# Performance work log

Measured on AMD Instinct MI355X. Metric: run time of the kernel, lower is better.

The kernel has to match this reference:

```python
import jax, jax.numpy as jnp
import numpy as np

QLEN, KLEN, BSZ, NHEAD, DHEAD = 1024, 1024, 2, 16, 64
RLEN = QLEN + KLEN
SCALE = 1.0 / np.sqrt(DHEAD).astype(np.float32)  # 1/sqrt(d_head)


def setup_inputs() -> dict:
    key = jax.random.key(0)
    ks = jax.random.split(key, 10)
    return {
        "q_head": jax.random.normal(ks[0], (QLEN, BSZ, NHEAD, DHEAD), jnp.float32),
        "k_head_h": jax.random.normal(ks[1], (KLEN, BSZ, NHEAD, DHEAD), jnp.float32),
        "v_head_h": jax.random.normal(ks[2], (KLEN, BSZ, NHEAD, DHEAD), jnp.float32),
        "k_head_r": jax.random.normal(ks[3], (RLEN, BSZ, NHEAD, DHEAD), jnp.float32),
        "seg_embed": jax.random.normal(ks[4], (2, NHEAD, DHEAD), jnp.float32),
        "seg_mat": jax.random.uniform(ks[5], (QLEN, KLEN, BSZ, 2), jnp.float32),
        "r_w_bias": jax.random.normal(ks[6], (NHEAD, DHEAD), jnp.float32),
        "r_r_bias": jax.random.normal(ks[7], (NHEAD, DHEAD), jnp.float32),
        "r_s_bias": jax.random.normal(ks[8], (NHEAD, DHEAD), jnp.float32),
        "attn_mask": jnp.zeros((QLEN, KLEN, 1, 1), jnp.float32),
    }


def _rel_shift(x, klen):
    # x: [qlen, rlen, bsz, n_head] -> [qlen, klen, bsz, n_head]
    x = jnp.transpose(x, (1, 0, 2, 3))[1:]          # drop first position row
    x = jnp.transpose(x, (1, 0, 2, 3))[:, :klen]    # keep first klen columns
    return x


def reference(q_head, k_head_h, v_head_h, k_head_r, seg_embed, seg_mat,
              r_w_bias, r_r_bias, r_s_bias, attn_mask):
    # content-based score
    ac = jnp.einsum('ibnd,jbnd->ijbn', q_head + r_w_bias, k_head_h)
    # position-based score with relative shift
    bd = jnp.einsum('ibnd,jbnd->ijbn', q_head + r_r_bias, k_head_r)
    bd = _rel_shift(bd, klen=ac.shape[1])
    # segment-based score
    ef = jnp.einsum('ibnd,snd->ibns', q_head + r_s_bias, seg_embed)
    ef = jnp.einsum('ijbs,ibns->ijbn', seg_mat, ef)
    attn_score = (ac + bd + ef) * SCALE
    attn_score = attn_score - 1e30 * attn_mask
    attn_prob = jax.nn.softmax(attn_score, axis=1)  # over key dim j
    attn_vec = jnp.einsum('ijbn,jbnd->ibnd', attn_prob, v_head_h)
    return attn_vec
```

## Files before the change

kernel.cpp:

```cpp
#include <hip/hip_runtime.h>

#define QLEN 1024
#define KLEN 1024
#define BSZ 2
#define NHEAD 16
#define DHEAD 64
#define RS 2048
#define BLK_I 64
#define BLK_J 32
#define NT32 (KLEN / BLK_J)
#define NBN (BSZ * NHEAD)

#define SC2f  0.18033688011112440f
#define MBIGf 1.4426950408889634e30f

#define SEGP_BYTES  16777216u
#define KT_BYTES    ((size_t)NBN * NT32 * 4096)

typedef __attribute__((ext_vector_type(8))) short s16x8;
typedef __attribute__((ext_vector_type(8))) unsigned short u16x8;
typedef __attribute__((ext_vector_type(4))) unsigned short u16x4;
typedef __attribute__((ext_vector_type(4))) float f32x4;
typedef __attribute__((ext_vector_type(2))) float f32x2;

__device__ __forceinline__ unsigned short f2bf(float f) {
    union { float f; unsigned int u; } x; x.f = f;
    unsigned int r = x.u + 0x7fffu + ((x.u >> 16) & 1u);
    return (unsigned short)(r >> 16);
}
__device__ __forceinline__ float bf2f(unsigned short h) {
    union { unsigned int u; float f; } x; x.u = ((unsigned int)h) << 16;
    return x.f;
}

typedef const __attribute__((address_space(1))) unsigned int* gas_t;
typedef __attribute__((address_space(3))) unsigned int* las_t;
__device__ __forceinline__ void gl_lds16(const void* g, void* l) {
    __builtin_amdgcn_global_load_lds((gas_t)g, (las_t)l, 16, 0, 0);
}

__global__ __launch_bounds__(256)
void pack_all_kernel(const float* __restrict__ segmat,
                     const float* __restrict__ mask,
                     const float* __restrict__ kh,
                     const float* __restrict__ kr,
                     const float* __restrict__ v,
                     u16x4* __restrict__ segP,
                     unsigned short* __restrict__ Kp,
                     unsigned short* __restrict__ Krp,
                     unsigned short* __restrict__ Vtp)
{
    __shared__ float VT[32][65];
    const int bid = blockIdx.x;
    const int tid = threadIdx.x;

    if (bid < 1024) {
        const int gid = bid * 256 + tid;
        const int j8  = gid & (KLEN / 8 - 1);
        const int i   = (gid >> 7) & (QLEN - 1);
        const int b   = gid >> 17;
        const float* sp = segmat + ((size_t)(i * KLEN + j8 * 8) * BSZ + b) * 2;
        const float* mp = mask + (size_t)i * KLEN + j8 * 8;
        u16x4* op = segP + (size_t)(b * QLEN + i) * KLEN + j8 * 8;
#pragma unroll
        for (int e = 0; e < 8; ++e) {
            const f32x2 sm = *(const f32x2*)(sp + e * (BSZ * 2));
            u16x4 pk;
            pk[0] = f2bf(sm[0]); pk[1] = f2bf(sm[1]);
            pk[2] = f2bf(mp[e] * MBIGf); pk[3] = 0;
            op[e] = pk;
        }
    } else {
        const int blk = bid - 1024;
        const int bn  = blk >> 5;
        const int jt  = blk & (NT32 - 1);
        const int b   = bn & 1;
        const int n   = bn >> 1;
        const int boff = b * NHEAD * DHEAD + n * DHEAD;
        const int j0  = jt * BLK_J;

        {
            const int j  = tid >> 3;
            const int dq = (tid & 7) * 8;
            const float* vp = v + (size_t)(j0 + j) * RS + boff + dq;
#pragma unroll
            for (int e = 0; e < 8; ++e) VT[j][dq + e] = vp[e];
        }
        __syncthreads();

        const size_t tb = (size_t)blk * 2048;
        {
            const int row = tid >> 3;
            const int ch  = (tid & 7) ^ (row & 7);
            u16x8 ok, orr;
            const float* hp = kh + (size_t)(j0 + row) * RS + boff + ch * 8;
            const float* rp = kr + (size_t)(j0 + row + 1) * RS + boff + ch * 8;
#pragma unroll
            for (int e = 0; e < 8; ++e) { ok[e] = f2bf(hp[e]); orr[e] = f2bf(rp[e]); }
            *(u16x8*)&Kp [tb + (size_t)tid * 8] = ok;
            *(u16x8*)&Krp[tb + (size_t)tid * 8] = orr;
        }
        {
            const int d  = tid >> 2;
            const int g  = tid & 3;
            const int ch = g ^ (d & 3);
            u16x8 ov;
#pragma unroll
            for (int e = 0; e < 8; ++e) ov[e] = f2bf(VT[ch * 8 + e][d]);
            *(u16x8*)&Vtp[tb + (size_t)tid * 8] = ov;
        }
    }
}

__global__ __launch_bounds__(256, 2)
void relattn_kernel(const float* __restrict__ q,
                    const float* __restrict__ segemb,
                    const float* __restrict__ rwb,
                    const float* __restrict__ rrb,
                    const float* __restrict__ rsb,
                    const u16x4* __restrict__ segP,
                    const unsigned short* __restrict__ Kp,
                    const unsigned short* __restrict__ Krp,
                    const unsigned short* __restrict__ Vtp,
                    float* __restrict__ out)
{
    __shared__ unsigned short KhL[2][32][64];
    __shared__ unsigned short KrL[2][32][64];
    __shared__ unsigned short VtL[2][64][32];
    __shared__ unsigned short PlP[4][16][40];

    const int F = blockIdx.x;
    const int x = F & 7;
    const int k = F >> 3;
    const int g = (k >> 4) * 8 + x;
    const int i0 = (g >> 1) * BLK_I;
    const int b  = g & 1;
    const int n  = k & 15;
    const int bn = n * 2 + b;
    const int boff = b * NHEAD * DHEAD + n * DHEAD;

    const int tid  = threadIdx.x;
    const int wave = tid >> 6;
    const int lane = tid & 63;
    const int q4   = lane >> 4;
    const int c    = lane & 15;
    const int iRow = i0 + wave * 16 + c;

    s16x8 qwf[2], qrf[2];
    float e0, e1;
    {
        const float* qp = q + (size_t)iRow * RS + boff;
        float es0 = 0.f, es1 = 0.f;
#pragma unroll
        for (int kk = 0; kk < 2; ++kk) {
            const int off = kk * 32 + q4 * 8;
            const f32x4 q0 = *(const f32x4*)(qp + off);
            const f32x4 q1 = *(const f32x4*)(qp + off + 4);
            const f32x4 w0 = *(const f32x4*)(rwb + n * DHEAD + off);
            const f32x4 w1 = *(const f32x4*)(rwb + n * DHEAD + off + 4);
            const f32x4 r0 = *(const f32x4*)(rrb + n * DHEAD + off);
            const f32x4 r1 = *(const f32x4*)(rrb + n * DHEAD + off + 4);
            const f32x4 sa = *(const f32x4*)(segemb + n * DHEAD + off);
            const f32x4 sb = *(const f32x4*)(segemb + n * DHEAD + off + 4);
            const f32x4 ta = *(const f32x4*)(segemb + (NHEAD + n) * DHEAD + off);
            const f32x4 tb = *(const f32x4*)(segemb + (NHEAD + n) * DHEAD + off + 4);
            const f32x4 ra = *(const f32x4*)(rsb + n * DHEAD + off);
            const f32x4 rb = *(const f32x4*)(rsb + n * DHEAD + off + 4);
            s16x8 tw, tr;
#pragma unroll
            for (int e = 0; e < 4; ++e) {
                tw[e]     = (short)f2bf(q0[e] + w0[e]);
                tw[4 + e] = (short)f2bf(q1[e] + w1[e]);
                tr[e]     = (short)f2bf(q0[e] + r0[e]);
                tr[4 + e] = (short)f2bf(q1[e] + r1[e]);
                es0 += (q0[e] + ra[e]) * sa[e] + (q1[e] + rb[e]) * sb[e];
                es1 += (q0[e] + ra[e]) * ta[e] + (q1[e] + rb[e]) * tb[e];
            }
            qwf[kk] = tw; qrf[kk] = tr;
        }
        es0 += __shfl_xor(es0, 16, 64); es0 += __shfl_xor(es0, 32, 64);
        es1 += __shfl_xor(es1, 16, 64); es1 += __shfl_xor(es1, 32, 64);
        e0 = es0 * SC2f; e1 = es1 * SC2f;
    }

    const int tbase = bn * NT32;
    auto stage = [&](int jt, int buf) {
        const size_t toff = ((size_t)(tbase + jt)) << 12;
        const int go = tid * 16;
        const int lo = wave * 1024;
        gl_lds16((const char*)Kp  + toff + go, (char*)&KhL[buf][0][0] + lo);
        gl_lds16((const char*)Krp + toff + go, (char*)&KrL[buf][0][0] + lo);
        gl_lds16((const char*)Vtp + toff + go, (char*)&VtL[buf][0][0] + lo);
    };

    stage(0, 0);
    __syncthreads();

    float m = -INFINITY, lsum = 0.f;
    f32x4 acc[4];
#pragma unroll
    for (int dt = 0; dt < 4; ++dt) acc[dt] = (f32x4)0.f;

    const u16x4* spB = segP + (size_t)b * QLEN * KLEN;
    int cur = 0;
    for (int jt = 0; jt < NT32; ++jt) {
        if (jt + 1 < NT32) stage(jt + 1, cur ^ 1);

        const int j0g = jt * BLK_J;
        u16x8 pg[2][2];
        {
            const u16x4* pp = spB + (size_t)iRow * KLEN + j0g + q4 * 4;
            pg[0][0] = *(const u16x8*)pp;
            pg[0][1] = *(const u16x8*)(pp + 2);
            pg[1][0] = *(const u16x8*)(pp + 16);
            pg[1][1] = *(const u16x8*)(pp + 18);
        }

        f32x4 sjT[2];
        sjT[0] = (f32x4)0.f; sjT[1] = (f32x4)0.f;
        __builtin_amdgcn_s_setprio(1);
#pragma unroll
        for (int kk = 0; kk < 2; ++kk)
#pragma unroll
            for (int js = 0; js < 2; ++js) {
                const int row = js * 16 + c;
                const int pcK = ((kk * 4 + q4) ^ (c & 7)) * 8;
                const s16x8 khf = *(const s16x8*)&KhL[cur][row][pcK];
                const s16x8 krf = *(const s16x8*)&KrL[cur][row][pcK];
                sjT[js] = __builtin_amdgcn_mfma_f32_16x16x32_bf16(khf, qwf[kk], sjT[js], 0, 0, 0);
                sjT[js] = __builtin_amdgcn_mfma_f32_16x16x32_bf16(krf, qrf[kk], sjT[js], 0, 0, 0);
            }
        __builtin_amdgcn_s_setprio(0);

        float sc8[8];
#pragma unroll
        for (int js = 0; js < 2; ++js)
#pragma unroll
            for (int r = 0; r < 4; ++r) {
                const u16x8 g2 = pg[js][r >> 1];
                const int bb = (r & 1) * 4;
                sc8[js * 4 + r] = sjT[js][r] * SC2f
                                  + bf2f(g2[bb]) * e0 + bf2f(g2[bb + 1]) * e1
                                  - bf2f(g2[bb + 2]);
            }
        float mt = fmaxf(
            fmaxf(fmaxf(sc8[0], sc8[1]), fmaxf(sc8[2], sc8[3])),
            fmaxf(fmaxf(sc8[4], sc8[5]), fmaxf(sc8[6], sc8[7])));
        mt = fmaxf(mt, __shfl_xor(mt, 16, 64));
        mt = fmaxf(mt, __shfl_xor(mt, 32, 64));
        const float mn  = fmaxf(m, mt);
        const float scl = __builtin_amdgcn_exp2f(m - mn);
        m = mn;
#pragma unroll
        for (int dt = 0; dt < 4; ++dt) acc[dt] *= scl;
        float p[8], ps = 0.f;
#pragma unroll
        for (int e = 0; e < 8; ++e) {
            p[e] = __builtin_amdgcn_exp2f(sc8[e] - m);
            ps += p[e];
        }
        lsum = lsum * scl + ps;

#pragma unroll
        for (int js = 0; js < 2; ++js) {
            unsigned int wlo, whi;
            asm("v_cvt_pk_bf16_f32 %0, %1, %2" : "=v"(wlo) : "v"(p[js * 4 + 0]), "v"(p[js * 4 + 1]));
            asm("v_cvt_pk_bf16_f32 %0, %1, %2" : "=v"(whi) : "v"(p[js * 4 + 2]), "v"(p[js * 4 + 3]));
            uint2 wv; wv.x = wlo; wv.y = whi;
            *(uint2*)((char*)&PlP[wave][c][0] + js * 32 + q4 * 8) = wv;
        }
        const s16x8 pf = *(const s16x8*)&PlP[wave][c][q4 * 8];

        __builtin_amdgcn_s_setprio(1);
#pragma unroll
        for (int dt = 0; dt < 4; ++dt) {
            const s16x8 vf = *(const s16x8*)&VtL[cur][dt * 16 + c][(q4 ^ (c & 3)) * 8];
            acc[dt] = __builtin_amdgcn_mfma_f32_16x16x32_bf16(vf, pf, acc[dt], 0, 0, 0);
        }
        __builtin_amdgcn_s_setprio(0);

        __syncthreads();
        cur ^= 1;
    }

    lsum += __shfl_xor(lsum, 16, 64);
    lsum += __shfl_xor(lsum, 32, 64);

    {
        const float inv = 1.f / lsum;
        float* op = out + (size_t)iRow * RS + boff;
#pragma unroll
        for (int dt = 0; dt < 4; ++dt) {
            const f32x4 o = acc[dt] * inv;
            *(f32x4*)&op[dt * 16 + q4 * 4] = o;
        }
    }
}

extern "C" void kernel_launch(void* const* d_in, const int* in_sizes, int n_in,
                              void* d_out, int out_size, void* d_ws, size_t ws_size,
                              hipStream_t stream) {
    const float* q   = (const float*)d_in[0];
    const float* kh  = (const float*)d_in[1];
    const float* v   = (const float*)d_in[2];
    const float* kr  = (const float*)d_in[3];
    const float* se  = (const float*)d_in[4];
    const float* sm  = (const float*)d_in[5];
    const float* rwb = (const float*)d_in[6];
    const float* rrb = (const float*)d_in[7];
    const float* rsb = (const float*)d_in[8];
    const float* msk = (const float*)d_in[9];
    float* out = (float*)d_out;

    char* wsb = (char*)d_ws;
    u16x4* segP = (u16x4*)wsb;
    unsigned short* Kp  = (unsigned short*)(wsb + SEGP_BYTES);
    unsigned short* Krp = (unsigned short*)(wsb + SEGP_BYTES + KT_BYTES);
    unsigned short* Vtp = (unsigned short*)(wsb + SEGP_BYTES + 2 * KT_BYTES);

    pack_all_kernel<<<1024 + NBN * NT32, 256, 0, stream>>>(sm, msk, kh, kr, v,
                                                           segP, Kp, Krp, Vtp);
    relattn_kernel<<<512, 256, 0, stream>>>(q, se, rwb, rrb, rsb, segP, Kp, Krp, Vtp, out);
}
```

Before: 69.12 us.

## Prefetch segment tile one step ahead and use partial vmcnt waits

Segment-probability loads for the next key tile are issued together with the next K/Kr/V LDS stage, using ping-pong register buffers. The full __syncthreads is replaced by s_waitcnt vmcnt(4) plus s_barrier, so the just-issued prefetch loads stay in flight across the barrier. The loop is unrolled by two to make the buffer index and register sets static. The risks are higher register pressure and reliance on exact vmcnt counting for correctness, and the last iteration issues a redundant load.

```diff
diff --git a/kernel.cpp b/kernel.cpp
--- a/kernel.cpp
+++ b/kernel.cpp
@@ -192,29 +192,35 @@
         gl_lds16((const char*)Krp + toff + go, (char*)&KrL[buf][0][0] + lo);
         gl_lds16((const char*)Vtp + toff + go, (char*)&VtL[buf][0][0] + lo);
     };
-
-    stage(0, 0);
-    __syncthreads();
+    const u16x4* spB = segP + (size_t)b * QLEN * KLEN;
+    auto segload = [&](int jt, u16x8 (&pg)[2][2]) {
+        const u16x4* pp = spB + (size_t)iRow * KLEN + jt * BLK_J + q4 * 4;
+        pg[0][0] = *(const u16x8*)pp;
+        pg[0][1] = *(const u16x8*)(pp + 2);
+        pg[1][0] = *(const u16x8*)(pp + 16);
+        pg[1][1] = *(const u16x8*)(pp + 18);
+    };
 
     float m = -INFINITY, lsum = 0.f;
     f32x4 acc[4];
 #pragma unroll
     for (int dt = 0; dt < 4; ++dt) acc[dt] = (f32x4)0.f;
 
-    const u16x4* spB = segP + (size_t)b * QLEN * KLEN;
-    int cur = 0;
-    for (int jt = 0; jt < NT32; ++jt) {
-        if (jt + 1 < NT32) stage(jt + 1, cur ^ 1);
-
-        const int j0g = jt * BLK_J;
-        u16x8 pg[2][2];
-        {
-            const u16x4* pp = spB + (size_t)iRow * KLEN + j0g + q4 * 4;
-            pg[0][0] = *(const u16x8*)pp;
-            pg[0][1] = *(const u16x8*)(pp + 2);
-            pg[1][0] = *(const u16x8*)(pp + 16);
-            pg[1][1] = *(const u16x8*)(pp + 18);
-        }
+    u16x8 pgA[2][2], pgB[2][2];
+    stage(0, 0);
+    __builtin_amdgcn_sched_barrier(0);
+    segload(0, pgA);
+    __builtin_amdgcn_sched_barrier(0);
+    asm volatile("s_waitcnt vmcnt(4)" ::: "memory");
+    __builtin_amdgcn_s_barrier();
+    __builtin_amdgcn_sched_barrier(0);
+
+    auto body = [&](int t, int bufc, u16x8 (&pgC)[2][2], u16x8 (&pgN)[2][2]) {
+        const int tn = (t + 1 < NT32) ? t + 1 : NT32 - 1;
+        stage(tn, bufc ^ 1);
+        __builtin_amdgcn_sched_barrier(0);
+        segload(tn, pgN);
+        __builtin_amdgcn_sched_barrier(0);
 
         f32x4 sjT[2];
         sjT[0] = (f32x4)0.f; sjT[1] = (f32x4)0.f;
@@ -225,8 +231,8 @@
             for (int js = 0; js < 2; ++js) {
                 const int row = js * 16 + c;
                 const int pcK = ((kk * 4 + q4) ^ (c & 7)) * 8;
-                const s16x8 khf = *(const s16x8*)&KhL[cur][row][pcK];
-                const s16x8 krf = *(const s16x8*)&KrL[cur][row][pcK];
+                const s16x8 khf = *(const s16x8*)&KhL[bufc][row][pcK];
+                const s16x8 krf = *(const s16x8*)&KrL[bufc][row][pcK];
                 sjT[js] = __builtin_amdgcn_mfma_f32_16x16x32_bf16(khf, qwf[kk], sjT[js], 0, 0, 0);
                 sjT[js] = __builtin_amdgcn_mfma_f32_16x16x32_bf16(krf, qrf[kk], sjT[js], 0, 0, 0);
             }
@@ -237,7 +243,7 @@
         for (int js = 0; js < 2; ++js)
 #pragma unroll
             for (int r = 0; r < 4; ++r) {
-                const u16x8 g2 = pg[js][r >> 1];
+                const u16x8 g2 = pgC[js][r >> 1];
                 const int bb = (r & 1) * 4;
                 sc8[js * 4 + r] = sjT[js][r] * SC2f
                                   + bf2f(g2[bb]) * e0 + bf2f(g2[bb + 1]) * e1
@@ -274,18 +280,24 @@
         __builtin_amdgcn_s_setprio(1);
 #pragma unroll
         for (int dt = 0; dt < 4; ++dt) {
-            const s16x8 vf = *(const s16x8*)&VtL[cur][dt * 16 + c][(q4 ^ (c & 3)) * 8];
+            const s16x8 vf = *(const s16x8*)&VtL[bufc][dt * 16 + c][(q4 ^ (c & 3)) * 8];
             acc[dt] = __builtin_amdgcn_mfma_f32_16x16x32_bf16(vf, pf, acc[dt], 0, 0, 0);
         }
         __builtin_amdgcn_s_setprio(0);
 
-        __syncthreads();
-        cur ^= 1;
+        asm volatile("s_waitcnt vmcnt(4)" ::: "memory");
+        __builtin_amdgcn_s_barrier();
+        __builtin_amdgcn_sched_barrier(0);
+    };
+
+    for (int o = 0; o < NT32 / 2; ++o) {
+        body(2 * o + 0, 0, pgA, pgB);
+        body(2 * o + 1, 1, pgB, pgA);
     }
+    asm volatile("s_waitcnt vmcnt(0)" ::: "memory");
 
     lsum += __shfl_xor(lsum, 16, 64);
     lsum += __shfl_xor(lsum, 32, 64);
-
     {
         const float inv = 1.f / lsum;
         float* op = out + (size_t)iRow * RS + boff;
```

Measured after the change: 70.29 us. About the same (+1.7%).

## Tile-pack segment/mask matrix into per-wave fragment order for coalesced loads

Applied to the files above, without the earlier changes.

The packing pass now reads seg_mat and mask in 16x32 tiles through shared memory. It writes bf16 segment weights and the mask term in an order that matches each wave's MFMA fragment layout, tiled per 16-row strip and 32-column block. The attention kernel then loads its per-tile segment data with contiguous lane-indexed 16-byte reads instead of strided row reads. The cost is extra shared-memory staging and twice as many pack blocks, and the index mapping must stay exactly consistent with the consumer's fragment layout.

```diff
diff --git a/kernel.cpp b/kernel.cpp
--- a/kernel.cpp
+++ b/kernel.cpp
@@ -45,33 +45,54 @@
                      const float* __restrict__ kh,
                      const float* __restrict__ kr,
                      const float* __restrict__ v,
-                     u16x4* __restrict__ segP,
+                     unsigned short* __restrict__ segT,
                      unsigned short* __restrict__ Kp,
                      unsigned short* __restrict__ Krp,
                      unsigned short* __restrict__ Vtp)
 {
+    __shared__ float smS[16][32][4];
+    __shared__ float smM[16][33];
     __shared__ float VT[32][65];
     const int bid = blockIdx.x;
     const int tid = threadIdx.x;
 
-    if (bid < 1024) {
-        const int gid = bid * 256 + tid;
-        const int j8  = gid & (KLEN / 8 - 1);
-        const int i   = (gid >> 7) & (QLEN - 1);
-        const int b   = gid >> 17;
-        const float* sp = segmat + ((size_t)(i * KLEN + j8 * 8) * BSZ + b) * 2;
-        const float* mp = mask + (size_t)i * KLEN + j8 * 8;
-        u16x4* op = segP + (size_t)(b * QLEN + i) * KLEN + j8 * 8;
-#pragma unroll
-        for (int e = 0; e < 8; ++e) {
-            const f32x2 sm = *(const f32x2*)(sp + e * (BSZ * 2));
-            u16x4 pk;
-            pk[0] = f2bf(sm[0]); pk[1] = f2bf(sm[1]);
-            pk[2] = f2bf(mp[e] * MBIGf); pk[3] = 0;
-            op[e] = pk;
+    if (bid < 2048) {
+        const int istrip = bid >> 5;
+        const int jt     = bid & 31;
+        const int ib     = istrip * 16;
+        const int jb     = jt * 32;
+        {
+            const int il = tid >> 4;
+            const int j2 = (tid & 15) * 2;
+            const float* sp = segmat + ((size_t)(ib + il) * KLEN + jb + j2) * 4;
+            *(f32x4*)&smS[il][j2][0]     = *(const f32x4*)sp;
+            *(f32x4*)&smS[il][j2 + 1][0] = *(const f32x4*)(sp + 4);
+            const float* mp = mask + (size_t)(ib + il) * KLEN + jb + j2;
+            smM[il][j2]     = mp[0] * MBIGf;
+            smM[il][j2 + 1] = mp[1] * MBIGf;
+        }
+        __syncthreads();
+        const int k  = tid >> 6;
+        const int l  = tid & 63;
+        const int q4 = l >> 4;
+        const int il = l & 15;
+        const int jl = (k >> 1) * 16 + q4 * 4 + (k & 1) * 2;
+#pragma unroll
+        for (int b = 0; b < 2; ++b) {
+            u16x8 o;
+#pragma unroll
+            for (int e = 0; e < 2; ++e) {
+                o[e * 4 + 0] = f2bf(smS[il][jl + e][b * 2]);
+                o[e * 4 + 1] = f2bf(smS[il][jl + e][b * 2 + 1]);
+                o[e * 4 + 2] = f2bf(smM[il][jl + e]);
+                o[e * 4 + 3] = 0;
+            }
+            unsigned short* op = segT + ((size_t)(b * 64 + istrip) << 16)
+                                 + (jt << 11) + tid * 8;
+            *(u16x8*)op = o;
         }
     } else {
-        const int blk = bid - 1024;
+        const int blk = bid - 2048;
         const int bn  = blk >> 5;
         const int jt  = blk & (NT32 - 1);
         const int b   = bn & 1;
@@ -118,7 +139,7 @@
                     const float* __restrict__ rwb,
                     const float* __restrict__ rrb,
                     const float* __restrict__ rsb,
-                    const u16x4* __restrict__ segP,
+                    const unsigned short* __restrict__ segT,
                     const unsigned short* __restrict__ Kp,
                     const unsigned short* __restrict__ Krp,
                     const unsigned short* __restrict__ Vtp,
@@ -201,20 +222,18 @@
 #pragma unroll
     for (int dt = 0; dt < 4; ++dt) acc[dt] = (f32x4)0.f;
 
-    const u16x4* spB = segP + (size_t)b * QLEN * KLEN;
+    const unsigned short* segW = segT + ((size_t)(b * 64 + (i0 >> 4) + wave) << 16);
+
     int cur = 0;
     for (int jt = 0; jt < NT32; ++jt) {
         if (jt + 1 < NT32) stage(jt + 1, cur ^ 1);
 
-        const int j0g = jt * BLK_J;
+        const unsigned short* st = segW + (jt << 11);
         u16x8 pg[2][2];
-        {
-            const u16x4* pp = spB + (size_t)iRow * KLEN + j0g + q4 * 4;
-            pg[0][0] = *(const u16x8*)pp;
-            pg[0][1] = *(const u16x8*)(pp + 2);
-            pg[1][0] = *(const u16x8*)(pp + 16);
-            pg[1][1] = *(const u16x8*)(pp + 18);
-        }
+        pg[0][0] = *(const u16x8*)(st + lane * 8);
+        pg[0][1] = *(const u16x8*)(st + 512 + lane * 8);
+        pg[1][0] = *(const u16x8*)(st + 1024 + lane * 8);
+        pg[1][1] = *(const u16x8*)(st + 1536 + lane * 8);
 
         f32x4 sjT[2];
         sjT[0] = (f32x4)0.f; sjT[1] = (f32x4)0.f;
@@ -313,12 +332,12 @@
     float* out = (float*)d_out;
 
     char* wsb = (char*)d_ws;
-    u16x4* segP = (u16x4*)wsb;
-    unsigned short* Kp  = (unsigned short*)(wsb + SEGP_BYTES);
-    unsigned short* Krp = (unsigned short*)(wsb + SEGP_BYTES + KT_BYTES);
-    unsigned short* Vtp = (unsigned short*)(wsb + SEGP_BYTES + 2 * KT_BYTES);
-
-    pack_all_kernel<<<1024 + NBN * NT32, 256, 0, stream>>>(sm, msk, kh, kr, v,
-                                                           segP, Kp, Krp, Vtp);
-    relattn_kernel<<<512, 256, 0, stream>>>(q, se, rwb, rrb, rsb, segP, Kp, Krp, Vtp, out);
-}
+    unsigned short* segT = (unsigned short*)wsb;
+    unsigned short* Kp   = (unsigned short*)(wsb + SEGP_BYTES);
+    unsigned short* Krp  = (unsigned short*)(wsb + SEGP_BYTES + KT_BYTES);
+    unsigned short* Vtp  = (unsigned short*)(wsb + SEGP_BYTES + 2 * KT_BYTES);
+
+    pack_all_kernel<<<2048 + NBN * NT32, 256, 0, stream>>>(sm, msk, kh, kr, v,
+                                                           segT, Kp, Krp, Vtp);
+    relattn_kernel<<<512, 256, 0, stream>>>(q, se, rwb, rrb, rsb, segT, Kp, Krp, Vtp, out);
+}
```

Result: faster. 56.10 us (-18.8%).
